# Optimization experiments

Hardware: AMD Instinct MI355X
Metric: run time of the kernel (lower is better)

Reference implementation:

```python
import jax, jax.numpy as jnp
import numpy as np

POINT_INFLUENCE = 1.0            # extent (sigma * grid_size)
KERNEL_RADIUS = 1.5 * POINT_INFLUENCE
N_KP = 15                        # n_kernel_points
DIM = 3
D_IN = 64
D_OUT = 64
N = 50000
M = 32
OFFSET_DIM = DIM * N_KP          # modulated=False


def setup_inputs() -> dict:
    key = jax.random.key(0)
    ks = jax.random.split(key, 8)
    query_points = jax.random.uniform(ks[0], (N, DIM), dtype=jnp.float32)
    support_points = jax.random.uniform(ks[1], (N, DIM), dtype=jnp.float32)
    neighbors = jax.random.randint(ks[2], (N, M), 0, N)
    x = jax.random.normal(ks[3], (N, D_IN), dtype=jnp.float32)
    # kernel point dispositions (load_kernels surrogate): center point fixed at 0,
    # remaining points inside the kernel ball of radius KERNEL_RADIUS
    kp = jax.random.uniform(ks[4], (N_KP, DIM), minval=-1.0, maxval=1.0, dtype=jnp.float32) * KERNEL_RADIUS
    K_points = kp.at[0].set(0.0)
    # xavier-normal-style params
    offset_weights = jax.random.normal(ks[5], (N_KP, D_IN, OFFSET_DIM), dtype=jnp.float32) * np.sqrt(2.0 / (D_IN + OFFSET_DIM))
    offset_bias = jnp.zeros((OFFSET_DIM,), dtype=jnp.float32)
    weight = jax.random.normal(ks[6], (N_KP, D_IN, D_OUT), dtype=jnp.float32) * np.sqrt(2.0 / (D_IN + D_OUT))
    return {
        "query_points": query_points,
        "support_points": support_points,
        "neighbors": neighbors,
        "x": x,
        "K_points": K_points,
        "offset_weights": offset_weights,
        "offset_bias": offset_bias,
        "weight": weight,
    }


def _kpconv_core(q, s, neigh, x, kpts, W, extent):
    """KPConv aggregation: kpts is [K,3] (rigid) or [N,K,3] (deformed)."""
    nb = s[neigh] - q[:, None, :]                          # [N,M,3] centered neighbors
    if kpts.ndim == 2:
        diff = nb[:, :, None, :] - kpts[None, None, :, :]  # [N,M,K,3]
    else:
        diff = nb[:, :, None, :] - kpts[:, None, :, :]     # [N,M,K,3]
    sqd = jnp.sum(diff * diff, axis=-1)                    # [N,M,K]
    # linear KP influence, aggregation_mode='sum'
    aw = jnp.maximum(1.0 - jnp.sqrt(sqd) / extent, 0.0)    # [N,M,K]
    aw = jnp.swapaxes(aw, 1, 2)                            # [N,K,M]
    nf = x[neigh]                                          # [N,M,Din]
    wf = jnp.einsum('nkm,nmd->nkd', aw, nf)                # [N,K,Din]
    return jnp.einsum('nkd,kde->ne', wf, W)                # [N,Dout]


def reference(query_points, support_points, neighbors, x, K_points, offset_weights, offset_bias, weight):
    # 1) rigid KPConv predicting per-query kernel-point offsets
    offset_feat = _kpconv_core(query_points, support_points, neighbors, x,
                               K_points, offset_weights, POINT_INFLUENCE) + offset_bias
    offsets = offset_feat.reshape(-1, N_KP, DIM) * POINT_INFLUENCE   # [N,K,3]
    # 2) deformable KPConv with per-query deformed kernel points
    deformed_K = K_points[None, :, :] + offsets                      # [N,K,3]
    new_feat = _kpconv_core(query_points, support_points, neighbors, x,
                            deformed_K, weight, POINT_INFLUENCE)
    return new_feat
```

## Files before the change

### kernel.cpp

```cpp
#include <hip/hip_runtime.h>

#define N_PTS 50000
#define M 32
#define KP 15
#define D 64
#define E1 45
#define P 16
#define WFS 1048
#define AWR 36
#define AWB 576

typedef __attribute__((ext_vector_type(8))) _Float16 f16x8;
typedef __attribute__((ext_vector_type(4))) float    f32x4;
typedef __attribute__((ext_vector_type(2))) _Float16 f16x2;
typedef __attribute__((ext_vector_type(2))) __fp16   fp16v2;

__device__ __forceinline__ unsigned pkrtz(float a, float b) {
    union { fp16v2 v; unsigned u; } x;
    x.v = __builtin_amdgcn_cvt_pkrtz(a, b);
    return x.u;
}
__device__ __forceinline__ unsigned pkrne(float a, float b) {
    union { f16x2 v; unsigned u; } x;
    x.v[0] = (_Float16)a; x.v[1] = (_Float16)b; return x.u;
}
__device__ __forceinline__ float h2f(unsigned bits16) {
    union { unsigned short s; _Float16 h; } x; x.s = (unsigned short)bits16;
    return (float)x.h;
}
__device__ __forceinline__ float fsqrt_fast(float x) {
#if __has_builtin(__builtin_amdgcn_sqrtf)
    return __builtin_amdgcn_sqrtf(x);
#else
    return sqrtf(x);
#endif
}
__device__ __forceinline__ void split2h(float a, float b, unsigned& hu, unsigned& lu) {
    hu = pkrtz(a, b);
    const float ra = a - h2f(hu & 0xffffu);
    const float rb = b - h2f(hu >> 16);
    lu = pkrtz(ra, rb);
}

#if defined(__HIP_DEVICE_COMPILE__) && __has_builtin(__builtin_amdgcn_perm)
__device__ __forceinline__ unsigned permb(unsigned a, unsigned b, unsigned sel) {
    return __builtin_amdgcn_perm(a, b, sel);
}
#else
__device__ __forceinline__ unsigned permb(unsigned a, unsigned b, unsigned sel) {
    if (sel == 0x05040100u) return (b & 0xffffu) | (a << 16);
    return (b >> 16) | (a & 0xffff0000u);
}
#endif

__global__ void prep_all(const float* __restrict__ x, const float* __restrict__ ow,
                         const float* __restrict__ w, unsigned* __restrict__ xw,
                         unsigned short* __restrict__ owh, unsigned short* __restrict__ owl,
                         unsigned short* __restrict__ wh)
{
    const int b = blockIdx.x, tid = threadIdx.x;
    if (b < 3125) {
        const int i = b * 256 + tid;
        const int n = i >> 4, c = i & 15;
        const float* src = x + n * 64 + c;
        uint2 u;
        u.x = pkrne(src[0],  src[16]);
        u.y = pkrne(src[32], src[48]);
        ((uint2*)xw)[i] = u;
    } else if (b < 3317) {
        const int t = (b - 3125) * 256 + tid;
        const int j = t & 7, lane = (t >> 3) & 63, rest = t >> 9;
        const int nt = rest % 3, ks = rest / 3;
        const int q = lane >> 4, c = lane & 15;
        const int pos  = ks * 32 + q * 8 + j;
        const int orig = pos ^ (((pos >> 6) & 3) << 2);
        const int d = orig >> 4, k = orig & 15, e = nt * 16 + c;
        const float v = (k < KP && e < E1) ? ow[k * (D * E1) + d * E1 + e] : 0.f;
        unsigned hu, lu; split2h(v, 0.f, hu, lu);
        owh[t] = (unsigned short)hu;
        owl[t] = (unsigned short)lu;
    } else {
        const int t = (b - 3317) * 256 + tid;
        const int j = t & 7, lane = (t >> 3) & 63, rest = t >> 9;
        const int nt = rest & 3, ks = rest >> 2;
        const int q = lane >> 4, c = lane & 15;
        const int pos = ks * 32 + q * 8 + j;
        const int k = pos >> 6, dsw = pos & 63;
        const int d = dsw ^ ((k & 7) << 3);
        const int e = nt * 16 + c;
        union { _Float16 h; unsigned short s; } cv;
        cv.h = (_Float16)w[k * (D * D) + d * D + e];
        wh[t] = cv.s;
    }
}

__global__ __launch_bounds__(512, 4) void kpconv_deform(
    const float* __restrict__ qpts, const float* __restrict__ spts,
    const int*   __restrict__ nbrs, const float* __restrict__ kpts,
    const float* __restrict__ obias,
    const unsigned* __restrict__ xw,
    const unsigned short* __restrict__ owh, const unsigned short* __restrict__ owl,
    const unsigned short* __restrict__ wh,
    float* __restrict__ out)
{
    __shared__ int   s_nbr[P][M];
    __shared__ float s_q[P][3];
    __shared__ float s_off[P][E1];
    __shared__ unsigned s_act[8];
    __shared__ __align__(16) unsigned short s_wfh[P][WFS];
    __shared__ __align__(16) char s_bufB[25088];
    unsigned short* s_awB = (unsigned short*)s_bufB;
    float (*s_part3)[16][49] = (float(*)[16][49])s_bufB;
    float (*s_red)[16][16]   = (float(*)[16][16])s_bufB;

    const int tid  = threadIdx.x;
    const int base = blockIdx.x * P;
    const int lane = tid & 63;
    const int wid  = tid >> 6;
    const int q    = lane >> 4, c = lane & 15;
    const int pg   = tid >> 5, mg = tid & 31;

    float nbx, nby, nbz;
    f16x8 fbh[2][4];

    if (tid < P * 3)  ((float*)s_q)[tid]  = qpts[base * 3 + tid];
    __syncthreads();

    {
        const int ni = nbrs[(base + pg) * M + mg];
        s_nbr[pg][mg] = ni;
        nbx = spts[ni * 3 + 0] - s_q[pg][0];
        nby = spts[ni * 3 + 1] - s_q[pg][1];
        nbz = spts[ni * 3 + 2] - s_q[pg][2];
        float av[16];
        av[15] = 0.f;
#pragma unroll
        for (int k = 0; k < KP; k++) {
            const float dx = nbx - kpts[k * 3 + 0];
            const float dy = nby - kpts[k * 3 + 1];
            const float dz = nbz - kpts[k * 3 + 2];
            av[k] = fmaxf(1.0f - fsqrt_fast(dx * dx + dy * dy + dz * dz), 0.f);
        }
        const int awb = pg * AWB + mg;
#pragma unroll
        for (int k2 = 0; k2 < 16; k2 += 2) {
            const unsigned hu = pkrne(av[k2], av[k2 + 1]);
            s_awB[awb + k2 * AWR]       = (unsigned short)hu;
            s_awB[awb + (k2 + 1) * AWR] = (unsigned short)(hu >> 16);
        }
    }

    {
        const int hc = c >> 2;
        const uint2* __restrict__ xwq = (const uint2*)xw;
#pragma unroll
        for (int pi = 0; pi < 2; pi++) {
            const int p = 2 * wid + pi;
            const int ab = p * AWB + (lane & 15) * AWR + q * 8;
            const f16x8 ah = *(const f16x8*)&s_awB[ab];
            uint2 g2[8];
#pragma unroll
            for (int j = 0; j < 8; j++)
                g2[j] = xwq[s_nbr[p][q * 8 + j] * 16 + c];
#pragma unroll
            for (int t = 0; t < 4; t++) {
                union { f16x8 v; unsigned u[4]; } bh;
#pragma unroll
                for (int jj = 0; jj < 4; jj++) {
                    const unsigned ga = (t < 2) ? g2[2 * jj + 1].x : g2[2 * jj + 1].y;
                    const unsigned gb = (t < 2) ? g2[2 * jj].x     : g2[2 * jj].y;
                    bh.u[jj] = permb(ga, gb, (t & 1) ? 0x07060302u : 0x05040100u);
                }
                fbh[pi][t] = bh.v;
                f32x4 dacc = {0.f, 0.f, 0.f, 0.f};
                dacc = __builtin_amdgcn_mfma_f32_16x16x32_f16(ah, bh.v, dacc, 0, 0, 0);
                const unsigned u01 = pkrne(dacc[0], dacc[1]);
                const unsigned u23 = pkrne(dacc[2], dacc[3]);
                const int eb = (t * 16 + c) * 16 + 4 * (q ^ hc);
                *(uint2*)&s_wfh[p][eb] = make_uint2(u01, u23);
            }
        }
    }
    __syncthreads();

    {
        const int pr = lane & 15;
        f32x4 acc0 = {0,0,0,0}, acc1 = {0,0,0,0}, acc2 = {0,0,0,0};
#pragma unroll
        for (int s = 0; s < 4; s++) {
            const int ks = wid * 4 + s;
            const f16x8 ahh = *(const f16x8*)&s_wfh[pr][ks * 32 + q * 8];
#pragma unroll
            for (int nt = 0; nt < 3; nt++) {
                const int f = ((ks * 3 + nt) * 64 + lane) * 8;
                const f16x8 bh = *(const f16x8*)&owh[f];
                const f16x8 bl = *(const f16x8*)&owl[f];
                f32x4* acc = (nt == 0) ? &acc0 : (nt == 1) ? &acc1 : &acc2;
                *acc = __builtin_amdgcn_mfma_f32_16x16x32_f16(ahh, bh, *acc, 0, 0, 0);
                *acc = __builtin_amdgcn_mfma_f32_16x16x32_f16(ahh, bl, *acc, 0, 0, 0);
            }
        }
#pragma unroll
        for (int r = 0; r < 4; r++) {
            s_part3[wid][4 * q + r][0 * 16 + c] = acc0[r];
            s_part3[wid][4 * q + r][1 * 16 + c] = acc1[r];
            s_part3[wid][4 * q + r][2 * 16 + c] = acc2[r];
        }
    }
    __syncthreads();

    for (int idx = tid; idx < P * E1; idx += 512) {
        const int p = idx / E1, e = idx % E1;
        float v = obias[e];
#pragma unroll
        for (int w8 = 0; w8 < 8; w8++)
            v += s_part3[w8][p][e];
        s_off[p][e] = v;
    }
    __syncthreads();

    {
        unsigned pmask = 0;
        float av[16];
        av[15] = 0.f;
#pragma unroll
        for (int k = 0; k < KP; k++) {
            const float kx = kpts[k * 3 + 0] + s_off[pg][3 * k + 0];
            const float ky = kpts[k * 3 + 1] + s_off[pg][3 * k + 1];
            const float kz = kpts[k * 3 + 2] + s_off[pg][3 * k + 2];
            const float dx = nbx - kx, dy = nby - ky, dz = nbz - kz;
            av[k] = fmaxf(1.0f - fsqrt_fast(dx * dx + dy * dy + dz * dz), 0.f);
            pmask |= (__ballot(av[k] > 0.f) ? 1u : 0u) << k;
        }
        const int awb = pg * AWB + mg;
#pragma unroll
        for (int k2 = 0; k2 < 16; k2 += 2) {
            const unsigned hu = pkrne(av[k2], av[k2 + 1]);
            s_awB[awb + k2 * AWR]       = (unsigned short)hu;
            s_awB[awb + (k2 + 1) * AWR] = (unsigned short)(hu >> 16);
        }
        if (lane == 0) s_act[wid] = pmask;
    }

    {
#pragma unroll
        for (int pi = 0; pi < 2; pi++) {
            const int p = 2 * wid + pi;
            const f16x8 awh_f = *(const f16x8*)&s_awB[p * AWB + (lane & 15) * AWR + q * 8];
#pragma unroll
            for (int t = 0; t < 4; t++) {
                f32x4 dacc = {0.f, 0.f, 0.f, 0.f};
                dacc = __builtin_amdgcn_mfma_f32_16x16x32_f16(fbh[pi][t], awh_f, dacc, 0, 0, 0);
                const unsigned u01 = pkrne(dacc[0], dacc[1]);
                const unsigned u23 = pkrne(dacc[2], dacc[3]);
                const int dsw = (t * 16 + 4 * q) ^ ((c & 7) << 3);
                *(uint2*)&s_wfh[p][c * 64 + dsw] = make_uint2(u01, u23);
            }
        }
    }
    __syncthreads();

    const unsigned u2 = s_act[0] | s_act[1] | s_act[2] | s_act[3] |
                        s_act[4] | s_act[5] | s_act[6] | s_act[7];

    {
        const int etile = wid & 3, kh = wid >> 2;
        const int pr = lane & 15;
        f32x4 acc = {0.f, 0.f, 0.f, 0.f};
#pragma unroll
        for (int k = 0; k < KP; k++) {
            if (!((u2 >> k) & 1)) continue;
            const int ks = k * 2 + kh;
            const f16x8 ah = *(const f16x8*)&s_wfh[pr][ks * 32 + q * 8];
            const f16x8 bh = *(const f16x8*)&wh[((ks * 4 + etile) * 64 + lane) * 8];
            acc = __builtin_amdgcn_mfma_f32_16x16x32_f16(ah, bh, acc, 0, 0, 0);
        }
        if (kh == 1) {
#pragma unroll
            for (int r = 0; r < 4; r++)
                s_red[etile][4 * q + r][c] = acc[r];
        }
        __syncthreads();
        if (kh == 0) {
#pragma unroll
            for (int r = 0; r < 4; r++)
                out[(base + 4 * q + r) * D + etile * 16 + c] =
                    acc[r] + s_red[etile][4 * q + r][c];
        }
    }
}

extern "C" void kernel_launch(void* const* d_in, const int* in_sizes, int n_in,
                              void* d_out, int out_size, void* d_ws, size_t ws_size,
                              hipStream_t stream) {
    const float* q   = (const float*)d_in[0];
    const float* s   = (const float*)d_in[1];
    const int*   nb  = (const int*)  d_in[2];
    const float* x   = (const float*)d_in[3];
    const float* kp  = (const float*)d_in[4];
    const float* ow  = (const float*)d_in[5];
    const float* ob  = (const float*)d_in[6];
    const float* w   = (const float*)d_in[7];
    float* out = (float*)d_out;

    unsigned*       xw  = (unsigned*)d_ws;
    unsigned short* owh = (unsigned short*)((char*)d_ws + 12800000);
    unsigned short* owl = (unsigned short*)((char*)d_ws + 12898304);
    unsigned short* wh  = (unsigned short*)((char*)d_ws + 12996608);

    prep_all<<<3557, 256, 0, stream>>>(x, ow, w, xw, owh, owl, wh);
    kpconv_deform<<<N_PTS / P, 512, 0, stream>>>(q, s, nb, kp, ob,
                                                 xw, owh, owl, wh, out);
}
```

Before: 157.0 us.

## Shrink LDS footprint with swizzled weights, 16-bit neighbor indices and buffer aliasing

```diff
diff --git a/kernel.cpp b/kernel.cpp
--- a/kernel.cpp
+++ b/kernel.cpp
@@ -6,9 +6,7 @@
 #define D 64
 #define E1 45
 #define P 16
-#define WFS 1048
-#define AWR 36
-#define AWB 576
+#define WFS 1032
 
 typedef __attribute__((ext_vector_type(8))) _Float16 f16x8;
 typedef __attribute__((ext_vector_type(4))) float    f32x4;
@@ -40,6 +38,12 @@
     const float ra = a - h2f(hu & 0xffffu);
     const float rb = b - h2f(hu >> 16);
     lu = pkrtz(ra, rb);
+}
+__device__ __forceinline__ int aw_w(int k, int m) {
+    return k * 32 + ((((m >> 3) ^ k) & 3) << 3) + (m & 7);
+}
+__device__ __forceinline__ int aw_r8(int row, int g) {
+    return row * 32 + (((g ^ row) & 3) << 3);
 }
 
 #if defined(__HIP_DEVICE_COMPILE__) && __has_builtin(__builtin_amdgcn_perm)
@@ -94,7 +98,7 @@
     }
 }
 
-__global__ __launch_bounds__(512, 4) void kpconv_deform(
+__global__ __launch_bounds__(512, 6) void kpconv_deform(
     const float* __restrict__ qpts, const float* __restrict__ spts,
     const int*   __restrict__ nbrs, const float* __restrict__ kpts,
     const float* __restrict__ obias,
@@ -103,15 +107,13 @@
     const unsigned short* __restrict__ wh,
     float* __restrict__ out)
 {
-    __shared__ int   s_nbr[P][M];
+    __shared__ __align__(16) unsigned short s_nbr[P][M];
     __shared__ float s_q[P][3];
     __shared__ float s_off[P][E1];
-    __shared__ unsigned s_act[8];
     __shared__ __align__(16) unsigned short s_wfh[P][WFS];
-    __shared__ __align__(16) char s_bufB[25088];
-    unsigned short* s_awB = (unsigned short*)s_bufB;
-    float (*s_part3)[16][49] = (float(*)[16][49])s_bufB;
-    float (*s_red)[16][16]   = (float(*)[16][16])s_bufB;
+    __shared__ __align__(16) unsigned short s_awB[P * 512];
+    float (*s_part3)[16][49] = (float(*)[16][49])s_wfh;
+    float (*s_red)[16][16]   = (float(*)[16][16])s_awB;
 
     const int tid  = threadIdx.x;
     const int base = blockIdx.x * P;
@@ -128,7 +130,7 @@
 
     {
         const int ni = nbrs[(base + pg) * M + mg];
-        s_nbr[pg][mg] = ni;
+        s_nbr[pg][mg] = (unsigned short)ni;
         nbx = spts[ni * 3 + 0] - s_q[pg][0];
         nby = spts[ni * 3 + 1] - s_q[pg][1];
         nbz = spts[ni * 3 + 2] - s_q[pg][2];
@@ -141,12 +143,12 @@
             const float dz = nbz - kpts[k * 3 + 2];
             av[k] = fmaxf(1.0f - fsqrt_fast(dx * dx + dy * dy + dz * dz), 0.f);
         }
-        const int awb = pg * AWB + mg;
+        const int awp = pg * 512;
 #pragma unroll
         for (int k2 = 0; k2 < 16; k2 += 2) {
             const unsigned hu = pkrne(av[k2], av[k2 + 1]);
-            s_awB[awb + k2 * AWR]       = (unsigned short)hu;
-            s_awB[awb + (k2 + 1) * AWR] = (unsigned short)(hu >> 16);
+            s_awB[awp + aw_w(k2, mg)]     = (unsigned short)hu;
+            s_awB[awp + aw_w(k2 + 1, mg)] = (unsigned short)(hu >> 16);
         }
     }
 
@@ -156,12 +158,11 @@
 #pragma unroll
         for (int pi = 0; pi < 2; pi++) {
             const int p = 2 * wid + pi;
-            const int ab = p * AWB + (lane & 15) * AWR + q * 8;
-            const f16x8 ah = *(const f16x8*)&s_awB[ab];
+            const f16x8 ah = *(const f16x8*)&s_awB[p * 512 + aw_r8(lane & 15, q)];
             uint2 g2[8];
 #pragma unroll
             for (int j = 0; j < 8; j++)
-                g2[j] = xwq[s_nbr[p][q * 8 + j] * 16 + c];
+                g2[j] = xwq[(int)s_nbr[p][q * 8 + j] * 16 + c];
 #pragma unroll
             for (int t = 0; t < 4; t++) {
                 union { f16x8 v; unsigned u[4]; } bh;
@@ -200,6 +201,7 @@
                 *acc = __builtin_amdgcn_mfma_f32_16x16x32_f16(ahh, bl, *acc, 0, 0, 0);
             }
         }
+        __syncthreads();
 #pragma unroll
         for (int r = 0; r < 4; r++) {
             s_part3[wid][4 * q + r][0 * 16 + c] = acc0[r];
@@ -232,21 +234,21 @@
             av[k] = fmaxf(1.0f - fsqrt_fast(dx * dx + dy * dy + dz * dz), 0.f);
             pmask |= (__ballot(av[k] > 0.f) ? 1u : 0u) << k;
         }
-        const int awb = pg * AWB + mg;
+        const int awp = pg * 512;
 #pragma unroll
         for (int k2 = 0; k2 < 16; k2 += 2) {
             const unsigned hu = pkrne(av[k2], av[k2 + 1]);
-            s_awB[awb + k2 * AWR]       = (unsigned short)hu;
-            s_awB[awb + (k2 + 1) * AWR] = (unsigned short)(hu >> 16);
-        }
-        if (lane == 0) s_act[wid] = pmask;
+            s_awB[awp + aw_w(k2, mg)]     = (unsigned short)hu;
+            s_awB[awp + aw_w(k2 + 1, mg)] = (unsigned short)(hu >> 16);
+        }
+        if (lane == 0) *(unsigned*)&s_wfh[wid][1024] = pmask;
     }
 
     {
 #pragma unroll
         for (int pi = 0; pi < 2; pi++) {
             const int p = 2 * wid + pi;
-            const f16x8 awh_f = *(const f16x8*)&s_awB[p * AWB + (lane & 15) * AWR + q * 8];
+            const f16x8 awh_f = *(const f16x8*)&s_awB[p * 512 + aw_r8(lane & 15, q)];
 #pragma unroll
             for (int t = 0; t < 4; t++) {
                 f32x4 dacc = {0.f, 0.f, 0.f, 0.f};
@@ -260,8 +262,9 @@
     }
     __syncthreads();
 
-    const unsigned u2 = s_act[0] | s_act[1] | s_act[2] | s_act[3] |
-                        s_act[4] | s_act[5] | s_act[6] | s_act[7];
+    unsigned u2 = 0;
+#pragma unroll
+    for (int w = 0; w < 8; w++) u2 |= *(const unsigned*)&s_wfh[w][1024];
 
     {
         const int etile = wid & 3, kh = wid >> 2;
```

Result: faster. 151.6 us (-3.4%).
